# Optimization experiments

Measured on AMD Instinct MI355X. Metric: run time of the kernel, lower is better.

Reference implementation:

```python
import jax, jax.numpy as jnp
import numpy as np

B, N = 4096, 128


def setup_inputs() -> dict:
    key = jax.random.key(0)
    X = jax.random.normal(key, (B, N, N), dtype=jnp.float32)
    # SPD batch: X X^T / N + eps*I guarantees strictly positive eigenvalues
    spd = jnp.einsum('bij,bkj->bik', X, X) / N + 1e-3 * jnp.eye(N, dtype=jnp.float32)[None]
    return {"input": spd}


def reference(input) -> jnp.ndarray:
    # Batched eigendecomposition (symmetric input -> eigh), then v @ diag(log e) @ v^T
    e, v = jnp.linalg.eigh(input)          # e: [B, N], v: [B, N, N]
    return jnp.einsum('bij,bj,bkj->bik', v, jnp.log(e), v)
```

## Files before the change

kernel.cpp:

```cpp
#include <hip/hip_runtime.h>
#include <hip/hip_bf16.h>
#include <math.h>

#define NM   128
#define PAD  132
#define PB   136

typedef __attribute__((ext_vector_type(8))) short bf16x8;
typedef __attribute__((ext_vector_type(4))) float f32x4;


__global__ __launch_bounds__(256,1)
void scale_kernel(const float* __restrict__ A, float* __restrict__ outY,
                  float* __restrict__ outM, float* __restrict__ lns)
{
    __shared__ __align__(16) float L[NM][PAD];
    __shared__ float rs[NM];
    __shared__ float s_inv;
    const int t = threadIdx.x;
    const long long b = blockIdx.x;
    const long long off = b << 14;
    for (int v = 0; v < 16; ++v) {
        int f = t + v*256;
        int row = f >> 5, c4 = (f & 31) << 2;
        *(float4*)&L[row][c4] = ((const float4*)(A + off))[f];
    }
    __syncthreads();
    if (t < NM) {
        float s = 0.f;
        for (int j = 0; j < NM; ++j) s += fabsf(L[t][j]);
        rs[t] = s;
    }
    __syncthreads();
    if (t < 64) {
        float m = fmaxf(rs[t], rs[t+64]);
        #pragma unroll
        for (int o = 32; o > 0; o >>= 1) m = fmaxf(m, __shfl_down(m, o, 64));
        if (t == 0) { s_inv = 1.0f/m; lns[b] = logf(m); }
    }
    __syncthreads();
    const float inv = s_inv;
    for (int v = 0; v < 16; ++v) {
        int f = t + v*256;
        int row = f >> 5, c4 = (f & 31) << 2;
        float4 x = *(const float4*)&L[row][c4];
        x.x *= inv; x.y *= inv; x.z *= inv; x.w *= inv;
        ((float4*)(outY + off))[f] = x;
        ((float4*)(outM + off))[f] = x;
    }
}

__global__ __launch_bounds__(256,1)
void rescale_kernel(const float* __restrict__ Sq, float* __restrict__ X,
                    float* __restrict__ M, float* __restrict__ lns)
{
    __shared__ __align__(16) float L[NM][PAD];
    __shared__ float rs[NM];
    __shared__ float s_g;
    const int t = threadIdx.x;
    const long long b = blockIdx.x;
    const long long off = b << 14;
    for (int v = 0; v < 16; ++v) {
        int f = t + v*256;
        int row = f >> 5, c4 = (f & 31) << 2;
        *(float4*)&L[row][c4] = ((const float4*)(Sq + off))[f];
    }
    __syncthreads();
    if (t < NM) {
        float s = 0.f;
        for (int j = 0; j < NM; ++j) s += fabsf(L[t][j]);
        rs[t] = s;
    }
    __syncthreads();
    if (t < 64) {
        float m = fmaxf(rs[t], rs[t+64]);
        #pragma unroll
        for (int o = 32; o > 0; o >>= 1) m = fmaxf(m, __shfl_down(m, o, 64));
        if (t == 0) { s_g = 1.0f/sqrtf(m); lns[b] = lns[b] + 0.5f*logf(m); }
    }
    __syncthreads();
    const float g = s_g;
    for (int v = 0; v < 16; ++v) {
        int f = t + v*256;
        float4 x = ((const float4*)(X + off))[f];
        x.x *= g; x.y *= g; x.z *= g; x.w *= g;
        ((float4*)(X + off))[f] = x;
        ((float4*)(M + off))[f] = x;
    }
}

__device__ __forceinline__ void tridec(int u, int &bi, int &bj) {
    int b = (int)(0.5f*(sqrtf(8.0f*(float)u + 1.0f) - 1.0f));
    while ((b+1)*(b+2)/2 <= u) ++b;
    while (b*(b+1)/2 > u) --b;
    bi = b; bj = u - b*(b+1)/2;
}

__global__ __launch_bounds__(512,1)
void gram_tri(const float* __restrict__ X, float* __restrict__ Out)
{
    __shared__ __align__(16) float LX[NM][PAD];
    const int t = threadIdx.x;
    const long long off = (long long)blockIdx.x << 14;
    for (int v = 0; v < 8; ++v) {
        int f = t + v*512;
        int row = f >> 5, c4 = (f & 31) << 2;
        *(float4*)&LX[row][c4] = ((const float4*)(X + off))[f];
    }
    __syncthreads();
    for (int u = t; u < 528; u += 512) {
        int bi, bj; tridec(u, bi, bj);
        const int r4 = bi << 2, c4 = bj << 2;
        float acc[4][4];
        #pragma unroll
        for (int i = 0; i < 4; ++i)
            #pragma unroll
            for (int j = 0; j < 4; ++j) acc[i][j] = 0.f;
        #pragma unroll 4
        for (int k = 0; k < NM; ++k) {
            float av[4], bv[4];
            *(float4*)av = *(const float4*)&LX[k][r4];
            *(float4*)bv = *(const float4*)&LX[k][c4];
            #pragma unroll
            for (int i = 0; i < 4; ++i)
                #pragma unroll
                for (int j = 0; j < 4; ++j) acc[i][j] = fmaf(av[i], bv[j], acc[i][j]);
        }
        #pragma unroll
        for (int i = 0; i < 4; ++i)
            *(float4*)&Out[off + (long long)(r4+i)*NM + c4] =
                make_float4(acc[i][0], acc[i][1], acc[i][2], acc[i][3]);
        if (bi != bj) {
            #pragma unroll
            for (int j = 0; j < 4; ++j)
                *(float4*)&Out[off + (long long)(c4+j)*NM + r4] =
                    make_float4(acc[0][j], acc[1][j], acc[2][j], acc[3][j]);
        }
    }
}

__device__ __forceinline__ void ns_tri_p1(const float (*LM)[PAD], const float (*LB)[PAD],
                                          float* __restrict__ outY, long long off,
                                          int bi, int bj, float a15, float a05)
{
    const int r4 = bi << 2, c4 = bj << 2;
    float acc[4][4];
    #pragma unroll
    for (int i = 0; i < 4; ++i)
        #pragma unroll
        for (int j = 0; j < 4; ++j) acc[i][j] = 0.f;
    #pragma unroll 4
    for (int k = 0; k < NM; ++k) {
        float av[4], bv[4];
        *(float4*)av = *(const float4*)&LB[k][r4];
        *(float4*)bv = *(const float4*)&LM[k][c4];
        #pragma unroll
        for (int i = 0; i < 4; ++i)
            #pragma unroll
            for (int j = 0; j < 4; ++j) acc[i][j] = fmaf(av[i], bv[j], acc[i][j]);
    }
    float o[4][4];
    #pragma unroll
    for (int i = 0; i < 4; ++i)
        #pragma unroll
        for (int j = 0; j < 4; ++j)
            o[i][j] = a15*LB[r4+i][c4+j] - a05*acc[i][j];
    if (bi == bj) {
        #pragma unroll
        for (int i = 0; i < 4; ++i)
            #pragma unroll
            for (int j = 0; j < 4; ++j)
                if (j > i) { float s = 0.5f*(o[i][j] + o[j][i]); o[i][j] = s; o[j][i] = s; }
    }
    #pragma unroll
    for (int i = 0; i < 4; ++i)
        *(float4*)&outY[off + (long long)(r4+i)*NM + c4] =
            make_float4(o[i][0], o[i][1], o[i][2], o[i][3]);
    if (bi != bj) {
        #pragma unroll
        for (int j = 0; j < 4; ++j)
            *(float4*)&outY[off + (long long)(c4+j)*NM + r4] =
                make_float4(o[0][j], o[1][j], o[2][j], o[3][j]);
    }
}

__device__ __forceinline__ void ns_tri_p2(const float (*LM)[PAD], float (*LB)[PAD],
                                          int bi, int bj)
{
    const int r4 = bi << 2, c4 = bj << 2;
    float acc[4][4];
    #pragma unroll
    for (int i = 0; i < 4; ++i)
        #pragma unroll
        for (int j = 0; j < 4; ++j) acc[i][j] = 0.f;
    #pragma unroll 4
    for (int k = 0; k < NM; ++k) {
        float av[4], bv[4];
        *(float4*)av = *(const float4*)&LM[k][r4];
        *(float4*)bv = *(const float4*)&LM[k][c4];
        #pragma unroll
        for (int i = 0; i < 4; ++i)
            #pragma unroll
            for (int j = 0; j < 4; ++j) acc[i][j] = fmaf(av[i], bv[j], acc[i][j]);
    }
    #pragma unroll
    for (int i = 0; i < 4; ++i)
        *(float4*)&LB[r4+i][c4] = make_float4(acc[i][0], acc[i][1], acc[i][2], acc[i][3]);
    if (bi != bj) {
        #pragma unroll
        for (int j = 0; j < 4; ++j)
            *(float4*)&LB[c4+j][r4] = make_float4(acc[0][j], acc[1][j], acc[2][j], acc[3][j]);
    }
}

__device__ __forceinline__ void ns_tri_p3(const float (*LM)[PAD], const float (*LB)[PAD],
                                          float* __restrict__ outM, long long off,
                                          int bi, int bj, float q)
{
    const int r4 = bi << 2, c4 = bj << 2;
    float acc[4][4];
    #pragma unroll
    for (int i = 0; i < 4; ++i)
        #pragma unroll
        for (int j = 0; j < 4; ++j) acc[i][j] = 0.f;
    #pragma unroll 4
    for (int k = 0; k < NM; ++k) {
        float av[4], bv[4];
        *(float4*)av = *(const float4*)&LM[k][r4];
        *(float4*)bv = *(const float4*)&LB[k][c4];
        #pragma unroll
        for (int i = 0; i < 4; ++i)
            #pragma unroll
            for (int j = 0; j < 4; ++j) acc[i][j] = fmaf(av[i], bv[j], acc[i][j]);
    }
    float o[4][4];
    #pragma unroll
    for (int i = 0; i < 4; ++i)
        #pragma unroll
        for (int j = 0; j < 4; ++j)
            o[i][j] = q*(9.f*LM[r4+i][c4+j] - 6.f*LB[r4+i][c4+j] + acc[i][j]);
    if (bi == bj) {
        #pragma unroll
        for (int i = 0; i < 4; ++i)
            #pragma unroll
            for (int j = 0; j < 4; ++j)
                if (j > i) { float s = 0.5f*(o[i][j] + o[j][i]); o[i][j] = s; o[j][i] = s; }
    }
    #pragma unroll
    for (int i = 0; i < 4; ++i)
        *(float4*)&outM[off + (long long)(r4+i)*NM + c4] =
            make_float4(o[i][0], o[i][1], o[i][2], o[i][3]);
    if (bi != bj) {
        #pragma unroll
        for (int j = 0; j < 4; ++j)
            *(float4*)&outM[off + (long long)(c4+j)*NM + r4] =
                make_float4(o[0][j], o[1][j], o[2][j], o[3][j]);
    }
}

__global__ __launch_bounds__(512,1)
void ns_tri(const float* __restrict__ Mp, const float* __restrict__ Yp,
            float* __restrict__ outM, float* __restrict__ outY,
            float cc, float dd)
{
    __shared__ __align__(16) float LM[NM][PAD];
    __shared__ __align__(16) float LB[NM][PAD];
    const int t = threadIdx.x;
    const long long off = (long long)blockIdx.x << 14;
    for (int v = 0; v < 8; ++v) {
        int f = t + v*512;
        int row = f >> 5, c4 = (f & 31) << 2;
        *(float4*)&LM[row][c4] = ((const float4*)(Mp + off))[f];
        *(float4*)&LB[row][c4] = ((const float4*)(Yp + off))[f];
    }
    __syncthreads();

    const float a15 = 1.5f*dd, a05 = 0.5f*dd, q = 0.25f*cc;
    int bi0, bj0, bi1 = -1, bj1 = 0;
    tridec(t, bi0, bj0);
    if (t < 16) tridec(512 + t, bi1, bj1);

    ns_tri_p1(LM, LB, outY, off, bi0, bj0, a15, a05);
    if (bi1 >= 0) ns_tri_p1(LM, LB, outY, off, bi1, bj1, a15, a05);
    __syncthreads();
    ns_tri_p2(LM, LB, bi0, bj0);
    if (bi1 >= 0) ns_tri_p2(LM, LB, bi1, bj1);
    __syncthreads();
    ns_tri_p3(LM, LB, outM, off, bi0, bj0, q);
    if (bi1 >= 0) ns_tri_p3(LM, LB, outM, off, bi1, bj1, q);
}

__device__ __forceinline__ f32x4 mfma16(bf16x8 a, bf16x8 b, f32x4 c) {
    return __builtin_amdgcn_mfma_f32_16x16x32_bf16(a, b, c, 0, 0, 0);
}

__device__ __forceinline__ void splitbf(float x, unsigned short &h, unsigned short &l) {
    __hip_bfloat16 bh = __float2bfloat16(x);
    float r = x - __bfloat162float(bh);
    __hip_bfloat16 bl = __float2bfloat16(r);
    h = *(unsigned short*)&bh;
    l = *(unsigned short*)&bl;
}

__device__ __forceinline__ float ldsM(const unsigned short* __restrict__ H,
                                      const unsigned short* __restrict__ L,
                                      int row, int col) {
    unsigned int uh = ((unsigned int)H[row*PB + col]) << 16;
    unsigned int ul = ((unsigned int)L[row*PB + col]) << 16;
    return __uint_as_float(uh) + __uint_as_float(ul);
}

__device__ __forceinline__ bf16x8 ldfrag(const unsigned short* __restrict__ a,
                                         int rb, int lane, int kc) {
    int row = rb*16 + (lane & 15);
    int col = kc*32 + ((lane >> 4) & 3)*8;
    return *(const bf16x8*)(a + row*PB + col);
}

__device__ __forceinline__ f32x4 symdiag(f32x4 a, int lane) {
    const int g = (lane >> 4) & 3, j = lane & 15;
    const int rp = j & 3;
    f32x4 out;
    #pragma unroll
    for (int r = 0; r < 4; ++r) {
        int lp = 4*g + r + ((j >> 2) << 4);
        float t0 = __shfl(a[0], lp, 64);
        float t1 = __shfl(a[1], lp, 64);
        float t2 = __shfl(a[2], lp, 64);
        float t3 = __shfl(a[3], lp, 64);
        float tv = (rp == 0) ? t0 : (rp == 1) ? t1 : (rp == 2) ? t2 : t3;
        out[r] = 0.5f*(a[r] + tv);
    }
    return out;
}

__device__ __forceinline__ void st_split(unsigned short* __restrict__ H,
                                         unsigned short* __restrict__ L,
                                         int Tr, int Tc, int lane, f32x4 o) {
    int col = Tc*16 + (lane & 15);
    int rb  = Tr*16 + ((lane >> 4) & 3)*4;
    #pragma unroll
    for (int r = 0; r < 4; ++r) {
        unsigned short h, l;
        splitbf(o[r], h, l);
        H[(rb+r)*PB + col] = h;
        L[(rb+r)*PB + col] = l;
        if (Tr != Tc) { H[col*PB + rb + r] = h; L[col*PB + rb + r] = l; }
    }
}

__device__ __forceinline__ void stg_sym(float* __restrict__ out, long long off,
                                        int Tr, int Tc, int lane, f32x4 o) {
    int col = Tc*16 + (lane & 15);
    int rb  = Tr*16 + ((lane >> 4) & 3)*4;
    #pragma unroll
    for (int r = 0; r < 4; ++r)
        out[off + (long long)(rb+r)*NM + col] = o[r];
    if (Tr != Tc)
        *(f32x4*)&out[off + (long long)col*NM + rb] = o;
}

__device__ __forceinline__ f32x4 yepi(const unsigned short* __restrict__ Yh,
                                      const unsigned short* __restrict__ Yl,
                                      int Tr, int Tc, int lane, f32x4 a,
                                      float a15, float a05) {
    int col = Tc*16 + (lane & 15);
    int rb  = Tr*16 + ((lane >> 4) & 3)*4;
    f32x4 o;
    #pragma unroll
    for (int r = 0; r < 4; ++r)
        o[r] = a15*ldsM(Yh, Yl, rb+r, col) - a05*a[r];
    if (Tr == Tc) o = symdiag(o, lane);
    return o;
}

__device__ __forceinline__ f32x4 mepi(const unsigned short* __restrict__ Mh,
                                      const unsigned short* __restrict__ Ml,
                                      const unsigned short* __restrict__ Th,
                                      const unsigned short* __restrict__ Tl,
                                      int Tr, int Tc, int lane, f32x4 a, float q) {
    int col = Tc*16 + (lane & 15);
    int rb  = Tr*16 + ((lane >> 4) & 3)*4;
    f32x4 o;
    #pragma unroll
    for (int r = 0; r < 4; ++r)
        o[r] = q*(9.f*ldsM(Mh, Ml, rb+r, col) - 6.f*ldsM(Th, Tl, rb+r, col) + a[r]);
    if (Tr == Tc) o = symdiag(o, lane);
    return o;
}

__device__ __forceinline__ f32x4 pepi(const unsigned short* __restrict__ Ph,
                                      const unsigned short* __restrict__ Pl,
                                      int Tr, int Tc, int lane, f32x4 a,
                                      float s1, float s2, float dadd) {
    int col = Tc*16 + (lane & 15);
    int rb  = Tr*16 + ((lane >> 4) & 3)*4;
    f32x4 o;
    #pragma unroll
    for (int r = 0; r < 4; ++r)
        o[r] = s1*a[r] - s2*ldsM(Ph, Pl, rb+r, col) + ((rb+r) == col ? dadd : 0.f);
    if (Tr == Tc) o = symdiag(o, lane);
    return o;
}

template<int W>
struct TileSet {
    static constexpr int P  = W & 3;
    static constexpr int R0 = P;
    static constexpr int R1 = 7 - P;
    static constexpr int H  = W >> 2;
    static constexpr int N  = (10 - H) / 2;
    static constexpr int tr(int i) { int g = 2*i + H; return g <= R0 ? R0 : R1; }
    static constexpr int tc(int i) { int g = 2*i + H; return g <= R0 ? g : g - R0 - 1; }
};

template<int W>
__device__ __forceinline__ void tri8_gemm(const unsigned short* __restrict__ Ah,
                                          const unsigned short* __restrict__ Al,
                                          const unsigned short* __restrict__ Bh,
                                          const unsigned short* __restrict__ Bl,
                                          int lane, f32x4* acc) {
    using TS = TileSet<W>;
    #pragma unroll
    for (int kc = 0; kc < 4; ++kc) {
        bf16x8 a0h = ldfrag(Ah, TS::R0, lane, kc), a0l = ldfrag(Al, TS::R0, lane, kc);
        bf16x8 a1h = ldfrag(Ah, TS::R1, lane, kc), a1l = ldfrag(Al, TS::R1, lane, kc);
        #pragma unroll
        for (int i = 0; i < TS::N; ++i) {
            const int r = TS::tr(i), c = TS::tc(i);
            bf16x8 bh = ldfrag(Bh, c, lane, kc), bl = ldfrag(Bl, c, lane, kc);
            bf16x8 ah = (r == TS::R0) ? a0h : a1h;
            bf16x8 al = (r == TS::R0) ? a0l : a1l;
            acc[i] = mfma16(ah, bh, acc[i]);
            acc[i] = mfma16(ah, bl, acc[i]);
            acc[i] = mfma16(al, bh, acc[i]);
        }
    }
}

template<int W>
__device__ __forceinline__ void ns_fused_body8(
    unsigned short* Mh, unsigned short* Ml,
    unsigned short* Yh, unsigned short* Yl,
    float* outY, long long off, int lane, int niter)
{
    using TS = TileSet<W>;
    constexpr int NT_ = TS::N;
    const f32x4 z = {0.f, 0.f, 0.f, 0.f};
    f32x4 acc[NT_], yv[NT_];

    for (int j = 0; j < niter; ++j) {
        const int last = (j == niter-1);
        const float cc = (j < niter-3) ? 1.5f : ((j == niter-3) ? 1.116f : 1.0f);
        const float dd = sqrtf(cc);
        const float a15 = 1.5f*dd, a05 = 0.5f*dd;

        #pragma unroll
        for (int i = 0; i < NT_; ++i) acc[i] = z;
        tri8_gemm<W>(Yh, Yl, Mh, Ml, lane, acc);
        #pragma unroll
        for (int i = 0; i < NT_; ++i)
            yv[i] = yepi(Yh, Yl, TS::tr(i), TS::tc(i), lane, acc[i], a15, a05);

        if (last) {
            #pragma unroll
            for (int i = 0; i < NT_; ++i)
                stg_sym(outY, off, TS::tr(i), TS::tc(i), lane, yv[i]);
            return;
        }
        __syncthreads();

        #pragma unroll
        for (int i = 0; i < NT_; ++i) acc[i] = z;
        tri8_gemm<W>(Mh, Ml, Mh, Ml, lane, acc);
        #pragma unroll
        for (int i = 0; i < NT_; ++i)
            st_split(Yh, Yl, TS::tr(i), TS::tc(i), lane, acc[i]);
        __syncthreads();

        #pragma unroll
        for (int i = 0; i < NT_; ++i) acc[i] = z;
        tri8_gemm<W>(Mh, Ml, Yh, Yl, lane, acc);
        const float q = 0.25f*cc;
        #pragma unroll
        for (int i = 0; i < NT_; ++i)
            acc[i] = mepi(Mh, Ml, Yh, Yl, TS::tr(i), TS::tc(i), lane, acc[i], q);
        __syncthreads();

        #pragma unroll
        for (int i = 0; i < NT_; ++i)
            st_split(Mh, Ml, TS::tr(i), TS::tc(i), lane, acc[i]);
        #pragma unroll
        for (int i = 0; i < NT_; ++i)
            st_split(Yh, Yl, TS::tr(i), TS::tc(i), lane, yv[i]);
        __syncthreads();
    }
}

__global__ __launch_bounds__(512,1)
void ns_fused(const float* __restrict__ Mp, const float* __restrict__ Yp,
              float* __restrict__ outY, int niter)
{
    __shared__ __align__(16) unsigned short pool[4*NM*PB];
    unsigned short* Mh = pool;
    unsigned short* Ml = pool + NM*PB;
    unsigned short* Yh = pool + 2*NM*PB;
    unsigned short* Yl = pool + 3*NM*PB;

    const int t = threadIdx.x;
    const long long off = (long long)blockIdx.x << 14;
    for (int v = 0; v < 8; ++v) {
        int f = t + v*512;
        int row = f >> 5, c4 = (f & 31) << 2;
        float4 x = ((const float4*)(Mp + off))[f];
        ushort4 h, l;
        splitbf(x.x, h.x, l.x); splitbf(x.y, h.y, l.y);
        splitbf(x.z, h.z, l.z); splitbf(x.w, h.w, l.w);
        *(ushort4*)&Mh[row*PB + c4] = h;
        *(ushort4*)&Ml[row*PB + c4] = l;
        x = ((const float4*)(Yp + off))[f];
        splitbf(x.x, h.x, l.x); splitbf(x.y, h.y, l.y);
        splitbf(x.z, h.z, l.z); splitbf(x.w, h.w, l.w);
        *(ushort4*)&Yh[row*PB + c4] = h;
        *(ushort4*)&Yl[row*PB + c4] = l;
    }
    __syncthreads();

    const int lane = t & 63;
    const int w = t >> 6;
    switch (w) {
        case 0:  ns_fused_body8<0>(Mh,Ml,Yh,Yl,outY,off,lane,niter); break;
        case 1:  ns_fused_body8<1>(Mh,Ml,Yh,Yl,outY,off,lane,niter); break;
        case 2:  ns_fused_body8<2>(Mh,Ml,Yh,Yl,outY,off,lane,niter); break;
        case 3:  ns_fused_body8<3>(Mh,Ml,Yh,Yl,outY,off,lane,niter); break;
        case 4:  ns_fused_body8<4>(Mh,Ml,Yh,Yl,outY,off,lane,niter); break;
        case 5:  ns_fused_body8<5>(Mh,Ml,Yh,Yl,outY,off,lane,niter); break;
        case 6:  ns_fused_body8<6>(Mh,Ml,Yh,Yl,outY,off,lane,niter); break;
        default: ns_fused_body8<7>(Mh,Ml,Yh,Yl,outY,off,lane,niter); break;
    }
}

struct PolyCoefs {
    float a, bd;
    float s1, s2;
    float c0,c1,c2,c3,c4,c5,c6,c7;
    float f1, f2, f3;
};

template<int W>
__device__ __forceinline__ void poly_fused_body8(
    const unsigned short* Xh, const unsigned short* Xl,
    unsigned short* Ph, unsigned short* Pl,
    float* Out, long long off, int lane, PolyCoefs pc, float lnsb)
{
    using TS = TileSet<W>;
    constexpr int NT_ = TS::N;
    const f32x4 z = {0.f, 0.f, 0.f, 0.f};
    f32x4 acc[NT_];

    for (int step = 0; step < 8; ++step) {
        #pragma unroll
        for (int i = 0; i < NT_; ++i) acc[i] = z;
        tri8_gemm<W>(Xh, Xl, Ph, Pl, lane, acc);
        float s3v;
        switch (step) {
            case 0: s3v = pc.c0; break;  case 1: s3v = pc.c1; break;
            case 2: s3v = pc.c2; break;  case 3: s3v = pc.c3; break;
            case 4: s3v = pc.c4; break;  case 5: s3v = pc.c5; break;
            case 6: s3v = pc.c6; break;  default: s3v = pc.c7; break;
        }
        #pragma unroll
        for (int i = 0; i < NT_; ++i)
            acc[i] = pepi(Ph, Pl, TS::tr(i), TS::tc(i), lane, acc[i], pc.s1, pc.s2, s3v);
        __syncthreads();
        #pragma unroll
        for (int i = 0; i < NT_; ++i)
            st_split(Ph, Pl, TS::tr(i), TS::tc(i), lane, acc[i]);
        __syncthreads();
    }
    #pragma unroll
    for (int i = 0; i < NT_; ++i) acc[i] = z;
    tri8_gemm<W>(Xh, Xl, Ph, Pl, lane, acc);
    const float dadd = pc.f3 + lnsb;
    #pragma unroll
    for (int i = 0; i < NT_; ++i) {
        f32x4 o = pepi(Ph, Pl, TS::tr(i), TS::tc(i), lane, acc[i], pc.f1, pc.f2, dadd);
        stg_sym(Out, off, TS::tr(i), TS::tc(i), lane, o);
    }
}

__global__ __launch_bounds__(512,1)
void poly_fused(const float* __restrict__ Xp, float* __restrict__ Out,
                const float* __restrict__ lns, PolyCoefs pc)
{
    __shared__ __align__(16) unsigned short pool[4*NM*PB];
    unsigned short* Xh = pool;
    unsigned short* Xl = pool + NM*PB;
    unsigned short* Ph = pool + 2*NM*PB;
    unsigned short* Pl = pool + 3*NM*PB;

    const int t = threadIdx.x;
    const long long b = blockIdx.x;
    const long long off = b << 14;
    for (int v = 0; v < 8; ++v) {
        int f = t + v*512;
        int row = f >> 5, c4 = (f & 31) << 2;
        float4 x = ((const float4*)(Xp + off))[f];
        float4 p;
        p.x = pc.a*x.x + ((c4+0)==row ? pc.bd : 0.f);
        p.y = pc.a*x.y + ((c4+1)==row ? pc.bd : 0.f);
        p.z = pc.a*x.z + ((c4+2)==row ? pc.bd : 0.f);
        p.w = pc.a*x.w + ((c4+3)==row ? pc.bd : 0.f);
        ushort4 h, l;
        splitbf(x.x, h.x, l.x); splitbf(x.y, h.y, l.y);
        splitbf(x.z, h.z, l.z); splitbf(x.w, h.w, l.w);
        *(ushort4*)&Xh[row*PB + c4] = h;
        *(ushort4*)&Xl[row*PB + c4] = l;
        splitbf(p.x, h.x, l.x); splitbf(p.y, h.y, l.y);
        splitbf(p.z, h.z, l.z); splitbf(p.w, h.w, l.w);
        *(ushort4*)&Ph[row*PB + c4] = h;
        *(ushort4*)&Pl[row*PB + c4] = l;
    }
    __syncthreads();

    const float lnsb = lns[b];
    const int lane = t & 63;
    const int w = t >> 6;
    switch (w) {
        case 0:  poly_fused_body8<0>(Xh,Xl,Ph,Pl,Out,off,lane,pc,lnsb); break;
        case 1:  poly_fused_body8<1>(Xh,Xl,Ph,Pl,Out,off,lane,pc,lnsb); break;
        case 2:  poly_fused_body8<2>(Xh,Xl,Ph,Pl,Out,off,lane,pc,lnsb); break;
        case 3:  poly_fused_body8<3>(Xh,Xl,Ph,Pl,Out,off,lane,pc,lnsb); break;
        case 4:  poly_fused_body8<4>(Xh,Xl,Ph,Pl,Out,off,lane,pc,lnsb); break;
        case 5:  poly_fused_body8<5>(Xh,Xl,Ph,Pl,Out,off,lane,pc,lnsb); break;
        case 6:  poly_fused_body8<6>(Xh,Xl,Ph,Pl,Out,off,lane,pc,lnsb); break;
        default: poly_fused_body8<7>(Xh,Xl,Ph,Pl,Out,off,lane,pc,lnsb); break;
    }
}

#define LDA  129
#define NT   512
#define MAX_SWEEPS 14

__global__ __launch_bounds__(NT, 1)
void logeig_jacobi(const float* __restrict__ in, float* __restrict__ out)
{
    __shared__ float A[NM][LDA];
    __shared__ float V[NM][LDA];
    __shared__ float rc[64], rs[64];
    __shared__ float logd[NM];
    __shared__ float roff[NT/64], rdia[NT/64];
    __shared__ int   s_done;

    const int t = threadIdx.x;
    const long long b = blockIdx.x;
    const float* __restrict__ Ain  = in  + (b << 14);
    float* __restrict__       Aout = out + (b << 14);

    for (int k = 0; k < (NM*NM)/NT; ++k) {
        int idx = t + k*NT;
        int i = idx >> 7, j = idx & 127;
        A[i][j] = Ain[idx];
        V[i][j] = (i == j) ? 1.0f : 0.0f;
    }
    __syncthreads();

    for (int sweep = 0; sweep < MAX_SWEEPS; ++sweep) {
        for (int r = 0; r < NM-1; ++r) {
            if (t < 64) {
                int m = t, p, q;
                if (m == 0) { p = NM-1; q = r; }
                else {
                    p = r + m;            if (p >= NM-1) p -= (NM-1);
                    q = r - m + (NM-1);   if (q >= NM-1) q -= (NM-1);
                }
                float app = A[p][p], aqq = A[q][q], apq = A[p][q];
                float c = 1.0f, s = 0.0f;
                if (fabsf(apq) > 1e-12f*(fabsf(app)+fabsf(aqq)) + 1e-32f) {
                    float tau = (aqq - app) * 0.5f / apq;
                    float tt  = 1.0f / (fabsf(tau) + sqrtf(fmaf(tau,tau,1.0f)));
                    tt = (tau < 0.0f) ? -tt : tt;
                    c = rsqrtf(fmaf(tt,tt,1.0f));
                    s = tt * c;
                }
                rc[m] = c; rs[m] = s;
            }
            __syncthreads();
            for (int k = 0; k < (2*64*NM)/NT; ++k) {
                int task = t + k*NT;
                int i   = task & 127;
                int m   = (task >> 7) & 63;
                int isV = task >> 13;
                int p, q;
                if (m == 0) { p = NM-1; q = r; }
                else {
                    p = r + m;            if (p >= NM-1) p -= (NM-1);
                    q = r - m + (NM-1);   if (q >= NM-1) q -= (NM-1);
                }
                float c = rc[m], s = rs[m];
                if (isV == 0) {
                    float x = A[i][p], y = A[i][q];
                    A[i][p] = c*x - s*y;
                    A[i][q] = s*x + c*y;
                } else {
                    float x = V[i][p], y = V[i][q];
                    V[i][p] = c*x - s*y;
                    V[i][q] = s*x + c*y;
                }
            }
            __syncthreads();
            for (int k = 0; k < (64*NM)/NT; ++k) {
                int task = t + k*NT;
                int j = task & 127;
                int m = task >> 7;
                int p, q;
                if (m == 0) { p = NM-1; q = r; }
                else {
                    p = r + m;            if (p >= NM-1) p -= (NM-1);
                    q = r - m + (NM-1);   if (q >= NM-1) q -= (NM-1);
                }
                float c = rc[m], s = rs[m];
                float x = A[p][j], y = A[q][j];
                A[p][j] = c*x - s*y;
                A[q][j] = s*x + c*y;
            }
            __syncthreads();
        }
        float off2 = 0.0f, dia2 = 0.0f;
        for (int k = 0; k < (NM*NM)/NT; ++k) {
            int idx = t + k*NT;
            int i = idx >> 7, j = idx & 127;
            float v = A[i][j];
            if (i == j) dia2 += v*v; else off2 += v*v;
        }
        #pragma unroll
        for (int o = 32; o > 0; o >>= 1) {
            off2 += __shfl_down(off2, o, 64);
            dia2 += __shfl_down(dia2, o, 64);
        }
        if ((t & 63) == 0) { roff[t >> 6] = off2; rdia[t >> 6] = dia2; }
        __syncthreads();
        if (t == 0) {
            float o2 = 0.0f, d2 = 0.0f;
            for (int w = 0; w < NT/64; ++w) { o2 += roff[w]; d2 += rdia[w]; }
            s_done = (o2 <= 1e-13f * d2) ? 1 : 0;
        }
        __syncthreads();
        if (s_done) break;
    }

    if (t < NM) logd[t] = logf(fmaxf(A[t][t], 1e-12f));
    __syncthreads();
    for (int kk = 0; kk < (NM*NM)/NT; ++kk) {
        int idx = t + kk*NT;
        int i = idx >> 7, k = idx & 127;
        A[i][k] = V[i][k] * logd[k];
    }
    __syncthreads();
    {
        int i  = t >> 2;
        int jb = t & 3;
        float acc[32];
        #pragma unroll
        for (int jj = 0; jj < 32; ++jj) acc[jj] = 0.0f;
        for (int kk = 0; kk < NM; ++kk) {
            int k = (kk + jb) & 127;
            float w = A[i][k];
            #pragma unroll
            for (int jj = 0; jj < 32; ++jj)
                acc[jj] = fmaf(w, V[jb*32 + jj][k], acc[jj]);
        }
        #pragma unroll
        for (int jj = 0; jj < 32; ++jj)
            Aout[i*NM + jb*32 + jj] = acc[jj];
    }
}

static void cheb_log_power(double lo, double up, int deg, double* p)
{
    const int NC = deg + 1;
    const int MN = 64;
    double mid = 0.5*(lo+up), hw = 0.5*(up-lo);
    double cc[32];
    for (int j = 0; j < NC; ++j) {
        double s = 0.0;
        for (int m = 0; m < MN; ++m) {
            double th = M_PI*(m+0.5)/MN;
            s += log(mid + hw*cos(th)) * cos(j*th);
        }
        cc[j] = 2.0*s/MN;
    }
    double Tp[32] = {0}, Tc[32] = {0}, Tn[32];
    for (int j = 0; j < NC; ++j) p[j] = 0.0;
    Tp[0] = 1.0;  p[0] += 0.5*cc[0];
    Tc[1] = 1.0;  p[1] += cc[1];
    for (int k = 2; k <= deg; ++k) {
        for (int j = 0; j < NC; ++j) Tn[j] = -Tp[j];
        for (int j = 1; j < NC; ++j) Tn[j] += 2.0*Tc[j-1];
        for (int j = 0; j < NC; ++j) { p[j] += cc[k]*Tn[j]; Tp[j] = Tc[j]; Tc[j] = Tn[j]; }
    }
}

extern "C" void kernel_launch(void* const* d_in, const int* in_sizes, int n_in,
                              void* d_out, int out_size, void* d_ws, size_t ws_size,
                              hipStream_t stream) {
    const float* in = (const float*)d_in[0];
    float* out = (float*)d_out;
    const int batch = in_sizes[0] >> 14;
    const size_t matBytes = (size_t)batch * NM * NM * 4;
    const size_t need = matBytes + (size_t)batch * 4;

    if (ws_size < need) {
        logeig_jacobi<<<batch, NT, 0, stream>>>(in, out);
        return;
    }

    float* Mbuf = (float*)d_ws;
    float* lns  = (float*)((char*)d_ws + matBytes);

    scale_kernel<<<batch, 256, 0, stream>>>(in, out, Mbuf, lns);
    gram_tri<<<batch, 512, 0, stream>>>(out, Mbuf);
    rescale_kernel<<<batch, 256, 0, stream>>>(Mbuf, out, Mbuf, lns);

    for (int j = 0; j < 4; ++j)
        ns_tri<<<batch, 512, 0, stream>>>(Mbuf, out, Mbuf, out,
                                          1.5f, sqrtf(1.5f));

    ns_fused<<<batch, 512, 0, stream>>>(Mbuf, out, out, 8);
    ns_fused<<<batch, 512, 0, stream>>>(out,  out, out, 8);
    ns_fused<<<batch, 512, 0, stream>>>(out,  out, out, 6);

    const double lo = 0.25, up = 1.002;
    const double mid = 0.5*(lo+up), hw = 0.5*(up-lo);
    double p[11];
    cheb_log_power(lo, up, 10, p);

    PolyCoefs pc;
    pc.a  = (float)(p[10]/hw);
    pc.bd = (float)(p[9] - p[10]*mid/hw);
    pc.s1 = (float)(1.0/hw);
    pc.s2 = (float)(mid/hw);
    pc.c0 = (float)p[8]; pc.c1 = (float)p[7]; pc.c2 = (float)p[6];
    pc.c3 = (float)p[5]; pc.c4 = (float)p[4]; pc.c5 = (float)p[3];
    pc.c6 = (float)p[2]; pc.c7 = (float)p[1];
    pc.f1 = (float)(8.0/hw);
    pc.f2 = (float)(8.0*mid/hw);
    pc.f3 = (float)(8.0*p[0]);

    poly_fused<<<batch, 512, 0, stream>>>(out, out, lns, pc);
}
```

Baseline: 7.296 ms.

## Fuse four NS iterations, double wavefronts per block, lower log polynomial degree

The four separate ns_tri launches are merged into one ns_tri4 kernel that keeps M and Y in LDS across iterations, so the global round trips between iterations go away. ns_fused and poly_fused now run with 1024 threads (16 wavefronts), each handling fewer 16x16 tiles, which raises MFMA parallelism per block. The Chebyshev log polynomial drops from degree 10 to degree 8, removing two GEMM steps from poly_fused. This trades some accuracy in the log approximation for less work, and it relies on the extra synchronisation and the 1024-thread register budget not hurting throughput.

```diff
diff --git a/kernel.cpp b/kernel.cpp
--- a/kernel.cpp
+++ b/kernel.cpp
@@ -139,9 +139,9 @@
     }
 }
 
-__device__ __forceinline__ void ns_tri_p1(const float (*LM)[PAD], const float (*LB)[PAD],
-                                          float* __restrict__ outY, long long off,
-                                          int bi, int bj, float a15, float a05)
+__device__ __forceinline__ void tri_p1_reg(const float (*LM)[PAD], const float (*LY)[PAD],
+                                           int bi, int bj, float a15, float a05,
+                                           float o[4][4])
 {
     const int r4 = bi << 2, c4 = bj << 2;
     float acc[4][4];
@@ -152,19 +152,18 @@
     #pragma unroll 4
     for (int k = 0; k < NM; ++k) {
         float av[4], bv[4];
-        *(float4*)av = *(const float4*)&LB[k][r4];
+        *(float4*)av = *(const float4*)&LY[k][r4];
         *(float4*)bv = *(const float4*)&LM[k][c4];
         #pragma unroll
         for (int i = 0; i < 4; ++i)
             #pragma unroll
             for (int j = 0; j < 4; ++j) acc[i][j] = fmaf(av[i], bv[j], acc[i][j]);
     }
-    float o[4][4];
     #pragma unroll
     for (int i = 0; i < 4; ++i)
         #pragma unroll
         for (int j = 0; j < 4; ++j)
-            o[i][j] = a15*LB[r4+i][c4+j] - a05*acc[i][j];
+            o[i][j] = a15*LY[r4+i][c4+j] - a05*acc[i][j];
     if (bi == bj) {
         #pragma unroll
         for (int i = 0; i < 4; ++i)
@@ -172,20 +171,10 @@
             for (int j = 0; j < 4; ++j)
                 if (j > i) { float s = 0.5f*(o[i][j] + o[j][i]); o[i][j] = s; o[j][i] = s; }
     }
-    #pragma unroll
-    for (int i = 0; i < 4; ++i)
-        *(float4*)&outY[off + (long long)(r4+i)*NM + c4] =
-            make_float4(o[i][0], o[i][1], o[i][2], o[i][3]);
-    if (bi != bj) {
-        #pragma unroll
-        for (int j = 0; j < 4; ++j)
-            *(float4*)&outY[off + (long long)(c4+j)*NM + r4] =
-                make_float4(o[0][j], o[1][j], o[2][j], o[3][j]);
-    }
-}
-
-__device__ __forceinline__ void ns_tri_p2(const float (*LM)[PAD], float (*LB)[PAD],
-                                          int bi, int bj)
+}
+
+__device__ __forceinline__ void tri_p2_lds(const float (*LM)[PAD], float (*LY)[PAD],
+                                           int bi, int bj)
 {
     const int r4 = bi << 2, c4 = bj << 2;
     float acc[4][4];
@@ -205,17 +194,16 @@
     }
     #pragma unroll
     for (int i = 0; i < 4; ++i)
-        *(float4*)&LB[r4+i][c4] = make_float4(acc[i][0], acc[i][1], acc[i][2], acc[i][3]);
+        *(float4*)&LY[r4+i][c4] = make_float4(acc[i][0], acc[i][1], acc[i][2], acc[i][3]);
     if (bi != bj) {
         #pragma unroll
         for (int j = 0; j < 4; ++j)
-            *(float4*)&LB[c4+j][r4] = make_float4(acc[0][j], acc[1][j], acc[2][j], acc[3][j]);
-    }
-}
-
-__device__ __forceinline__ void ns_tri_p3(const float (*LM)[PAD], const float (*LB)[PAD],
-                                          float* __restrict__ outM, long long off,
-                                          int bi, int bj, float q)
+            *(float4*)&LY[c4+j][r4] = make_float4(acc[0][j], acc[1][j], acc[2][j], acc[3][j]);
+    }
+}
+
+__device__ __forceinline__ void tri_p3_reg(const float (*LM)[PAD], const float (*LY)[PAD],
+                                           int bi, int bj, float q, float o[4][4])
 {
     const int r4 = bi << 2, c4 = bj << 2;
     float acc[4][4];
@@ -227,18 +215,17 @@
     for (int k = 0; k < NM; ++k) {
         float av[4], bv[4];
         *(float4*)av = *(const float4*)&LM[k][r4];
-        *(float4*)bv = *(const float4*)&LB[k][c4];
+        *(float4*)bv = *(const float4*)&LY[k][c4];
         #pragma unroll
         for (int i = 0; i < 4; ++i)
             #pragma unroll
             for (int j = 0; j < 4; ++j) acc[i][j] = fmaf(av[i], bv[j], acc[i][j]);
     }
-    float o[4][4];
     #pragma unroll
     for (int i = 0; i < 4; ++i)
         #pragma unroll
         for (int j = 0; j < 4; ++j)
-            o[i][j] = q*(9.f*LM[r4+i][c4+j] - 6.f*LB[r4+i][c4+j] + acc[i][j]);
+            o[i][j] = q*(9.f*LM[r4+i][c4+j] - 6.f*LY[r4+i][c4+j] + acc[i][j]);
     if (bi == bj) {
         #pragma unroll
         for (int i = 0; i < 4; ++i)
@@ -246,48 +233,67 @@
             for (int j = 0; j < 4; ++j)
                 if (j > i) { float s = 0.5f*(o[i][j] + o[j][i]); o[i][j] = s; o[j][i] = s; }
     }
+}
+
+__device__ __forceinline__ void tri_wb(float (*L)[PAD], int bi, int bj, const float o[4][4])
+{
+    const int r4 = bi << 2, c4 = bj << 2;
     #pragma unroll
     for (int i = 0; i < 4; ++i)
-        *(float4*)&outM[off + (long long)(r4+i)*NM + c4] =
-            make_float4(o[i][0], o[i][1], o[i][2], o[i][3]);
+        *(float4*)&L[r4+i][c4] = make_float4(o[i][0], o[i][1], o[i][2], o[i][3]);
     if (bi != bj) {
         #pragma unroll
         for (int j = 0; j < 4; ++j)
-            *(float4*)&outM[off + (long long)(c4+j)*NM + r4] =
-                make_float4(o[0][j], o[1][j], o[2][j], o[3][j]);
+            *(float4*)&L[c4+j][r4] = make_float4(o[0][j], o[1][j], o[2][j], o[3][j]);
     }
 }
 
 __global__ __launch_bounds__(512,1)
-void ns_tri(const float* __restrict__ Mp, const float* __restrict__ Yp,
-            float* __restrict__ outM, float* __restrict__ outY,
-            float cc, float dd)
+void ns_tri4(const float* __restrict__ Mp, const float* __restrict__ Yp,
+             float* __restrict__ outM, float* __restrict__ outY, int niter)
 {
     __shared__ __align__(16) float LM[NM][PAD];
-    __shared__ __align__(16) float LB[NM][PAD];
+    __shared__ __align__(16) float LY[NM][PAD];
     const int t = threadIdx.x;
     const long long off = (long long)blockIdx.x << 14;
     for (int v = 0; v < 8; ++v) {
         int f = t + v*512;
         int row = f >> 5, c4 = (f & 31) << 2;
         *(float4*)&LM[row][c4] = ((const float4*)(Mp + off))[f];
-        *(float4*)&LB[row][c4] = ((const float4*)(Yp + off))[f];
-    }
-    __syncthreads();
-
+        *(float4*)&LY[row][c4] = ((const float4*)(Yp + off))[f];
+    }
+    __syncthreads();
+
+    int b0i, b0j, b1i = -1, b1j = 0;
+    tridec(t, b0i, b0j);
+    if (t < 16) tridec(512 + t, b1i, b1j);
+
+    const float cc = 1.5f, dd = sqrtf(1.5f);
     const float a15 = 1.5f*dd, a05 = 0.5f*dd, q = 0.25f*cc;
-    int bi0, bj0, bi1 = -1, bj1 = 0;
-    tridec(t, bi0, bj0);
-    if (t < 16) tridec(512 + t, bi1, bj1);
-
-    ns_tri_p1(LM, LB, outY, off, bi0, bj0, a15, a05);
-    if (bi1 >= 0) ns_tri_p1(LM, LB, outY, off, bi1, bj1, a15, a05);
-    __syncthreads();
-    ns_tri_p2(LM, LB, bi0, bj0);
-    if (bi1 >= 0) ns_tri_p2(LM, LB, bi1, bj1);
-    __syncthreads();
-    ns_tri_p3(LM, LB, outM, off, bi0, bj0, q);
-    if (bi1 >= 0) ns_tri_p3(LM, LB, outM, off, bi1, bj1, q);
+    float y0[4][4], y1[4][4], m0[4][4], m1[4][4];
+
+    for (int it = 0; it < niter; ++it) {
+        tri_p1_reg(LM, LY, b0i, b0j, a15, a05, y0);
+        if (b1i >= 0) tri_p1_reg(LM, LY, b1i, b1j, a15, a05, y1);
+        __syncthreads();
+        tri_p2_lds(LM, LY, b0i, b0j);
+        if (b1i >= 0) tri_p2_lds(LM, LY, b1i, b1j);
+        __syncthreads();
+        tri_p3_reg(LM, LY, b0i, b0j, q, m0);
+        if (b1i >= 0) tri_p3_reg(LM, LY, b1i, b1j, q, m1);
+        __syncthreads();
+        tri_wb(LM, b0i, b0j, m0);
+        tri_wb(LY, b0i, b0j, y0);
+        if (b1i >= 0) { tri_wb(LM, b1i, b1j, m1); tri_wb(LY, b1i, b1j, y1); }
+        __syncthreads();
+    }
+
+    for (int v = 0; v < 8; ++v) {
+        int f = t + v*512;
+        int row = f >> 5, c4 = (f & 31) << 2;
+        ((float4*)(outM + off))[f] = *(const float4*)&LM[row][c4];
+        ((float4*)(outY + off))[f] = *(const float4*)&LY[row][c4];
+    }
 }
 
 __device__ __forceinline__ f32x4 mfma16(bf16x8 a, bf16x8 b, f32x4 c) {
@@ -404,23 +410,24 @@
 }
 
 template<int W>
-struct TileSet {
-    static constexpr int P  = W & 3;
+struct TS16 {
+    static constexpr int P  = W >> 2;
+    static constexpr int Q  = W & 3;
     static constexpr int R0 = P;
     static constexpr int R1 = 7 - P;
-    static constexpr int H  = W >> 2;
-    static constexpr int N  = (10 - H) / 2;
-    static constexpr int tr(int i) { int g = 2*i + H; return g <= R0 ? R0 : R1; }
-    static constexpr int tc(int i) { int g = 2*i + H; return g <= R0 ? g : g - R0 - 1; }
+    static constexpr int N  = (Q == 0) ? 3 : 2;
+    static constexpr int g(int i)  { return 4*i + Q; }
+    static constexpr int tr(int i) { return g(i) <= R0 ? R0 : R1; }
+    static constexpr int tc(int i) { return g(i) <= R0 ? g(i) : g(i) - R0 - 1; }
 };
 
 template<int W>
-__device__ __forceinline__ void tri8_gemm(const unsigned short* __restrict__ Ah,
-                                          const unsigned short* __restrict__ Al,
-                                          const unsigned short* __restrict__ Bh,
-                                          const unsigned short* __restrict__ Bl,
-                                          int lane, f32x4* acc) {
-    using TS = TileSet<W>;
+__device__ __forceinline__ void tri16_gemm(const unsigned short* __restrict__ Ah,
+                                           const unsigned short* __restrict__ Al,
+                                           const unsigned short* __restrict__ Bh,
+                                           const unsigned short* __restrict__ Bl,
+                                           int lane, f32x4* acc) {
+    using TS = TS16<W>;
     #pragma unroll
     for (int kc = 0; kc < 4; ++kc) {
         bf16x8 a0h = ldfrag(Ah, TS::R0, lane, kc), a0l = ldfrag(Al, TS::R0, lane, kc);
@@ -439,12 +446,12 @@
 }
 
 template<int W>
-__device__ __forceinline__ void ns_fused_body8(
+__device__ __forceinline__ void ns_fused_body16(
     unsigned short* Mh, unsigned short* Ml,
     unsigned short* Yh, unsigned short* Yl,
     float* outY, long long off, int lane, int niter)
 {
-    using TS = TileSet<W>;
+    using TS = TS16<W>;
     constexpr int NT_ = TS::N;
     const f32x4 z = {0.f, 0.f, 0.f, 0.f};
     f32x4 acc[NT_], yv[NT_];
@@ -457,7 +464,7 @@
 
         #pragma unroll
         for (int i = 0; i < NT_; ++i) acc[i] = z;
-        tri8_gemm<W>(Yh, Yl, Mh, Ml, lane, acc);
+        tri16_gemm<W>(Yh, Yl, Mh, Ml, lane, acc);
         #pragma unroll
         for (int i = 0; i < NT_; ++i)
             yv[i] = yepi(Yh, Yl, TS::tr(i), TS::tc(i), lane, acc[i], a15, a05);
@@ -472,7 +479,7 @@
 
         #pragma unroll
         for (int i = 0; i < NT_; ++i) acc[i] = z;
-        tri8_gemm<W>(Mh, Ml, Mh, Ml, lane, acc);
+        tri16_gemm<W>(Mh, Ml, Mh, Ml, lane, acc);
         #pragma unroll
         for (int i = 0; i < NT_; ++i)
             st_split(Yh, Yl, TS::tr(i), TS::tc(i), lane, acc[i]);
@@ -480,7 +487,7 @@
 
         #pragma unroll
         for (int i = 0; i < NT_; ++i) acc[i] = z;
-        tri8_gemm<W>(Mh, Ml, Yh, Yl, lane, acc);
+        tri16_gemm<W>(Mh, Ml, Yh, Yl, lane, acc);
         const float q = 0.25f*cc;
         #pragma unroll
         for (int i = 0; i < NT_; ++i)
@@ -497,7 +504,7 @@
     }
 }
 
-__global__ __launch_bounds__(512,1)
+__global__ __launch_bounds__(1024,1)
 void ns_fused(const float* __restrict__ Mp, const float* __restrict__ Yp,
               float* __restrict__ outY, int niter)
 {
@@ -509,8 +516,8 @@
 
     const int t = threadIdx.x;
     const long long off = (long long)blockIdx.x << 14;
-    for (int v = 0; v < 8; ++v) {
-        int f = t + v*512;
+    for (int v = 0; v < 4; ++v) {
+        int f = t + v*1024;
         int row = f >> 5, c4 = (f & 31) << 2;
         float4 x = ((const float4*)(Mp + off))[f];
         ushort4 h, l;
@@ -529,45 +536,52 @@
     const int lane = t & 63;
     const int w = t >> 6;
     switch (w) {
-        case 0:  ns_fused_body8<0>(Mh,Ml,Yh,Yl,outY,off,lane,niter); break;
-        case 1:  ns_fused_body8<1>(Mh,Ml,Yh,Yl,outY,off,lane,niter); break;
-        case 2:  ns_fused_body8<2>(Mh,Ml,Yh,Yl,outY,off,lane,niter); break;
-        case 3:  ns_fused_body8<3>(Mh,Ml,Yh,Yl,outY,off,lane,niter); break;
-        case 4:  ns_fused_body8<4>(Mh,Ml,Yh,Yl,outY,off,lane,niter); break;
-        case 5:  ns_fused_body8<5>(Mh,Ml,Yh,Yl,outY,off,lane,niter); break;
-        case 6:  ns_fused_body8<6>(Mh,Ml,Yh,Yl,outY,off,lane,niter); break;
-        default: ns_fused_body8<7>(Mh,Ml,Yh,Yl,outY,off,lane,niter); break;
+        case 0:  ns_fused_body16<0>(Mh,Ml,Yh,Yl,outY,off,lane,niter); break;
+        case 1:  ns_fused_body16<1>(Mh,Ml,Yh,Yl,outY,off,lane,niter); break;
+        case 2:  ns_fused_body16<2>(Mh,Ml,Yh,Yl,outY,off,lane,niter); break;
+        case 3:  ns_fused_body16<3>(Mh,Ml,Yh,Yl,outY,off,lane,niter); break;
+        case 4:  ns_fused_body16<4>(Mh,Ml,Yh,Yl,outY,off,lane,niter); break;
+        case 5:  ns_fused_body16<5>(Mh,Ml,Yh,Yl,outY,off,lane,niter); break;
+        case 6:  ns_fused_body16<6>(Mh,Ml,Yh,Yl,outY,off,lane,niter); break;
+        case 7:  ns_fused_body16<7>(Mh,Ml,Yh,Yl,outY,off,lane,niter); break;
+        case 8:  ns_fused_body16<8>(Mh,Ml,Yh,Yl,outY,off,lane,niter); break;
+        case 9:  ns_fused_body16<9>(Mh,Ml,Yh,Yl,outY,off,lane,niter); break;
+        case 10: ns_fused_body16<10>(Mh,Ml,Yh,Yl,outY,off,lane,niter); break;
+        case 11: ns_fused_body16<11>(Mh,Ml,Yh,Yl,outY,off,lane,niter); break;
+        case 12: ns_fused_body16<12>(Mh,Ml,Yh,Yl,outY,off,lane,niter); break;
+        case 13: ns_fused_body16<13>(Mh,Ml,Yh,Yl,outY,off,lane,niter); break;
+        case 14: ns_fused_body16<14>(Mh,Ml,Yh,Yl,outY,off,lane,niter); break;
+        default: ns_fused_body16<15>(Mh,Ml,Yh,Yl,outY,off,lane,niter); break;
     }
 }
 
 struct PolyCoefs {
     float a, bd;
     float s1, s2;
-    float c0,c1,c2,c3,c4,c5,c6,c7;
+    float c0,c1,c2,c3,c4,c5;
     float f1, f2, f3;
 };
 
 template<int W>
-__device__ __forceinline__ void poly_fused_body8(
+__device__ __forceinline__ void poly_fused_body16(
     const unsigned short* Xh, const unsigned short* Xl,
     unsigned short* Ph, unsigned short* Pl,
     float* Out, long long off, int lane, PolyCoefs pc, float lnsb)
 {
-    using TS = TileSet<W>;
+    using TS = TS16<W>;
     constexpr int NT_ = TS::N;
     const f32x4 z = {0.f, 0.f, 0.f, 0.f};
     f32x4 acc[NT_];
 
-    for (int step = 0; step < 8; ++step) {
+    for (int step = 0; step < 6; ++step) {
         #pragma unroll
         for (int i = 0; i < NT_; ++i) acc[i] = z;
-        tri8_gemm<W>(Xh, Xl, Ph, Pl, lane, acc);
+        tri16_gemm<W>(Xh, Xl, Ph, Pl, lane, acc);
         float s3v;
         switch (step) {
             case 0: s3v = pc.c0; break;  case 1: s3v = pc.c1; break;
             case 2: s3v = pc.c2; break;  case 3: s3v = pc.c3; break;
-            case 4: s3v = pc.c4; break;  case 5: s3v = pc.c5; break;
-            case 6: s3v = pc.c6; break;  default: s3v = pc.c7; break;
+            case 4: s3v = pc.c4; break;  default: s3v = pc.c5; break;
         }
         #pragma unroll
         for (int i = 0; i < NT_; ++i)
@@ -580,7 +594,7 @@
     }
     #pragma unroll
     for (int i = 0; i < NT_; ++i) acc[i] = z;
-    tri8_gemm<W>(Xh, Xl, Ph, Pl, lane, acc);
+    tri16_gemm<W>(Xh, Xl, Ph, Pl, lane, acc);
     const float dadd = pc.f3 + lnsb;
     #pragma unroll
     for (int i = 0; i < NT_; ++i) {
@@ -589,7 +603,7 @@
     }
 }
 
-__global__ __launch_bounds__(512,1)
+__global__ __launch_bounds__(1024,1)
 void poly_fused(const float* __restrict__ Xp, float* __restrict__ Out,
                 const float* __restrict__ lns, PolyCoefs pc)
 {
@@ -602,8 +616,8 @@
     const int t = threadIdx.x;
     const long long b = blockIdx.x;
     const long long off = b << 14;
-    for (int v = 0; v < 8; ++v) {
-        int f = t + v*512;
+    for (int v = 0; v < 4; ++v) {
+        int f = t + v*1024;
         int row = f >> 5, c4 = (f & 31) << 2;
         float4 x = ((const float4*)(Xp + off))[f];
         float4 p;
@@ -627,14 +641,22 @@
     const int lane = t & 63;
     const int w = t >> 6;
     switch (w) {
-        case 0:  poly_fused_body8<0>(Xh,Xl,Ph,Pl,Out,off,lane,pc,lnsb); break;
-        case 1:  poly_fused_body8<1>(Xh,Xl,Ph,Pl,Out,off,lane,pc,lnsb); break;
-        case 2:  poly_fused_body8<2>(Xh,Xl,Ph,Pl,Out,off,lane,pc,lnsb); break;
-        case 3:  poly_fused_body8<3>(Xh,Xl,Ph,Pl,Out,off,lane,pc,lnsb); break;
-        case 4:  poly_fused_body8<4>(Xh,Xl,Ph,Pl,Out,off,lane,pc,lnsb); break;
-        case 5:  poly_fused_body8<5>(Xh,Xl,Ph,Pl,Out,off,lane,pc,lnsb); break;
-        case 6:  poly_fused_body8<6>(Xh,Xl,Ph,Pl,Out,off,lane,pc,lnsb); break;
-        default: poly_fused_body8<7>(Xh,Xl,Ph,Pl,Out,off,lane,pc,lnsb); break;
+        case 0:  poly_fused_body16<0>(Xh,Xl,Ph,Pl,Out,off,lane,pc,lnsb); break;
+        case 1:  poly_fused_body16<1>(Xh,Xl,Ph,Pl,Out,off,lane,pc,lnsb); break;
+        case 2:  poly_fused_body16<2>(Xh,Xl,Ph,Pl,Out,off,lane,pc,lnsb); break;
+        case 3:  poly_fused_body16<3>(Xh,Xl,Ph,Pl,Out,off,lane,pc,lnsb); break;
+        case 4:  poly_fused_body16<4>(Xh,Xl,Ph,Pl,Out,off,lane,pc,lnsb); break;
+        case 5:  poly_fused_body16<5>(Xh,Xl,Ph,Pl,Out,off,lane,pc,lnsb); break;
+        case 6:  poly_fused_body16<6>(Xh,Xl,Ph,Pl,Out,off,lane,pc,lnsb); break;
+        case 7:  poly_fused_body16<7>(Xh,Xl,Ph,Pl,Out,off,lane,pc,lnsb); break;
+        case 8:  poly_fused_body16<8>(Xh,Xl,Ph,Pl,Out,off,lane,pc,lnsb); break;
+        case 9:  poly_fused_body16<9>(Xh,Xl,Ph,Pl,Out,off,lane,pc,lnsb); break;
+        case 10: poly_fused_body16<10>(Xh,Xl,Ph,Pl,Out,off,lane,pc,lnsb); break;
+        case 11: poly_fused_body16<11>(Xh,Xl,Ph,Pl,Out,off,lane,pc,lnsb); break;
+        case 12: poly_fused_body16<12>(Xh,Xl,Ph,Pl,Out,off,lane,pc,lnsb); break;
+        case 13: poly_fused_body16<13>(Xh,Xl,Ph,Pl,Out,off,lane,pc,lnsb); break;
+        case 14: poly_fused_body16<14>(Xh,Xl,Ph,Pl,Out,off,lane,pc,lnsb); break;
+        default: poly_fused_body16<15>(Xh,Xl,Ph,Pl,Out,off,lane,pc,lnsb); break;
     }
 }
 
@@ -822,30 +844,27 @@
     gram_tri<<<batch, 512, 0, stream>>>(out, Mbuf);
     rescale_kernel<<<batch, 256, 0, stream>>>(Mbuf, out, Mbuf, lns);
 
-    for (int j = 0; j < 4; ++j)
-        ns_tri<<<batch, 512, 0, stream>>>(Mbuf, out, Mbuf, out,
-                                          1.5f, sqrtf(1.5f));
-
-    ns_fused<<<batch, 512, 0, stream>>>(Mbuf, out, out, 8);
-    ns_fused<<<batch, 512, 0, stream>>>(out,  out, out, 8);
-    ns_fused<<<batch, 512, 0, stream>>>(out,  out, out, 6);
+    ns_tri4<<<batch, 512, 0, stream>>>(Mbuf, out, Mbuf, out, 4);
+
+    ns_fused<<<batch, 1024, 0, stream>>>(Mbuf, out, out, 8);
+    ns_fused<<<batch, 1024, 0, stream>>>(out,  out, out, 8);
+    ns_fused<<<batch, 1024, 0, stream>>>(out,  out, out, 6);
 
     const double lo = 0.25, up = 1.002;
     const double mid = 0.5*(lo+up), hw = 0.5*(up-lo);
-    double p[11];
-    cheb_log_power(lo, up, 10, p);
+    double p[9];
+    cheb_log_power(lo, up, 8, p);
 
     PolyCoefs pc;
-    pc.a  = (float)(p[10]/hw);
-    pc.bd = (float)(p[9] - p[10]*mid/hw);
+    pc.a  = (float)(p[8]/hw);
+    pc.bd = (float)(p[7] - p[8]*mid/hw);
     pc.s1 = (float)(1.0/hw);
     pc.s2 = (float)(mid/hw);
-    pc.c0 = (float)p[8]; pc.c1 = (float)p[7]; pc.c2 = (float)p[6];
-    pc.c3 = (float)p[5]; pc.c4 = (float)p[4]; pc.c5 = (float)p[3];
-    pc.c6 = (float)p[2]; pc.c7 = (float)p[1];
+    pc.c0 = (float)p[6]; pc.c1 = (float)p[5]; pc.c2 = (float)p[4];
+    pc.c3 = (float)p[3]; pc.c4 = (float)p[2]; pc.c5 = (float)p[1];
     pc.f1 = (float)(8.0/hw);
     pc.f2 = (float)(8.0*mid/hw);
     pc.f3 = (float)(8.0*p[0]);
 
-    poly_fused<<<batch, 512, 0, stream>>>(out, out, lns, pc);
-}
+    poly_fused<<<batch, 1024, 0, stream>>>(out, out, lns, pc);
+}
```

After: 7.207 ms. Within noise of the previous version (-1.2%).
